# Optimization experiments

Hardware: AMD Instinct MI355X
Metric: run time of the kernel (lower is better)

## Reference

```python
import jax, jax.numpy as jnp
import numpy as np

B, N, D = 256, 256, 256
DELTA_BEARING = 5.0
DELTA_HEADING = 5.0
N_HEAD = int(360 / DELTA_HEADING)   # 72
N_BEAR = int(360 / DELTA_BEARING)   # 72
DOMAIN_PARAM = 2.0
EPS = 1e-14


def setup_inputs() -> dict:
    key = jax.random.key(0)
    ks = jax.random.split(key, 8)
    hidden_state = jax.random.normal(ks[0], (B, N, D), dtype=jnp.float32)
    distance_matrix = jax.random.uniform(ks[1], (B, N, N), dtype=jnp.float32) * 10.0
    bearing_matrix = jax.random.uniform(ks[2], (B, N, N), dtype=jnp.float32) * 360.0
    heading_matrix = jax.random.uniform(ks[3], (B, N, N), dtype=jnp.float32) * 360.0
    sequence_mask = (jax.random.uniform(ks[4], (B, N)) > 0.1).astype(jnp.float32)
    domain = jnp.full((N_HEAD, N_BEAR), DOMAIN_PARAM, dtype=jnp.float32)
    lim = 1.0 / np.sqrt(2 * D)
    W = jax.random.uniform(ks[5], (D, 2 * D), minval=-lim, maxval=lim, dtype=jnp.float32)
    b = jax.random.uniform(ks[6], (D,), minval=-lim, maxval=lim, dtype=jnp.float32)
    return {"hidden_state": hidden_state, "distance_matrix": distance_matrix,
            "bearing_matrix": bearing_matrix, "heading_matrix": heading_matrix,
            "sequence_mask": sequence_mask, "domain": domain, "W": W, "b": b}


def _compute_weights(domain, distance_matrix, bearing_matrix, heading_matrix, sequence_mask):
    # domain lookup indices from heading/bearing bins
    idx1 = jnp.clip(jnp.floor((heading_matrix + DELTA_HEADING / 2) / DELTA_HEADING), 0, N_HEAD - 1).astype(jnp.int32)
    idx2 = jnp.clip(jnp.floor((bearing_matrix + DELTA_BEARING / 2) / DELTA_BEARING), 0, N_BEAR - 1).astype(jnp.int32)
    w = jax.nn.relu(domain[idx1, idx2] - distance_matrix)  # (B,N,N)
    # pairwise sequence mask and no-self-attention mask
    wm = sequence_mask[:, :, None] * sequence_mask[:, None, :]  # (B,N,N)
    ped = 1.0 - jnp.eye(w.shape[1], dtype=w.dtype)               # (N,N)
    valid = (ped[None, :, :] * wm) > 0
    w = jnp.where(valid, w, 0.0)
    # masked softmax over dim=2: zeros are treated as masked, epsilon-stabilized
    mask = (w != 0).astype(w.dtype)
    masked_exps = jnp.exp(w) * mask + EPS
    w = masked_exps / (masked_exps.sum(axis=2, keepdims=True) + EPS)
    return jnp.where(valid, w, 0.0)


def reference(hidden_state, distance_matrix, bearing_matrix, heading_matrix, sequence_mask, domain, W, b):
    weights = _compute_weights(domain, distance_matrix, bearing_matrix, heading_matrix, sequence_mask)
    weighted_hidden = jnp.einsum('bij,bjd->bid', weights, hidden_state)  # (B,N,D)
    cat = jnp.concatenate([weighted_hidden, hidden_state], axis=-1)       # (B,N,2D)
    return jnp.einsum('bnk,dk->bnd', cat, W) + b
```

## Files before the change

kernel.cpp:

```cpp
#include <hip/hip_runtime.h>
#include <hip/hip_bf16.h>


typedef __attribute__((ext_vector_type(4))) float  f32x4;
typedef __attribute__((ext_vector_type(8))) short  bf16x8;
typedef __attribute__((ext_vector_type(4))) short  bf16x4;

#define EPSC 1e-14f

__device__ __forceinline__ short f2bf(float v) {
  __hip_bfloat16 h = __float2bfloat16(v);
  return *reinterpret_cast<short*>(&h);
}
__device__ __forceinline__ void gload16(const void* g, void* l) {
  __builtin_amdgcn_global_load_lds(
      (const __attribute__((address_space(1))) void*)g,
      (__attribute__((address_space(3))) void*)l, 16, 0, 0);
}
__device__ __forceinline__ bf16x8 cvt8(const float* p) {
  f32x4 a = *(const f32x4*)p;
  f32x4 b = *(const f32x4*)(p + 4);
  bf16x8 r;
  r[0] = f2bf(a[0]); r[1] = f2bf(a[1]); r[2] = f2bf(a[2]); r[3] = f2bf(a[3]);
  r[4] = f2bf(b[0]); r[5] = f2bf(b[1]); r[6] = f2bf(b[2]); r[7] = f2bf(b[3]);
  return r;
}

__global__ void k0_pack(const float* __restrict__ W, short* __restrict__ Wbf) {
  int idx = blockIdx.x * 256 + threadIdx.x;
  f32x4 v = *(const f32x4*)(W + (size_t)idx * 4);
  bf16x4 pk;
  pk[0] = f2bf(v[0]); pk[1] = f2bf(v[1]); pk[2] = f2bf(v[2]); pk[3] = f2bf(v[3]);
  *(bf16x4*)(Wbf + (size_t)idx * 4) = pk;
}

__global__ void k0_check(const float* __restrict__ domain, float* __restrict__ flag) {
  __shared__ int s_ok[4];
  const int t = threadIdx.x;
  float v0 = domain[0];
  bool ok = true;
  for (int x = t; x < 72 * 72; x += 256) ok = ok && (domain[x] == v0);
  unsigned long long m = __ballot(ok);
  if ((t & 63) == 0) s_ok[t >> 6] = (m == ~0ull) ? 1 : 0;
  __syncthreads();
  if (t == 0) {
    flag[0] = v0;
    flag[1] = (s_ok[0] && s_ok[1] && s_ok[2] && s_ok[3]) ? 1.f : 0.f;
  }
}

__global__ __launch_bounds__(256) void k2a_weights(
    const float* __restrict__ dist, const float* __restrict__ bear,
    const float* __restrict__ head, const float* __restrict__ seqmask,
    const float* __restrict__ domain, const float* __restrict__ uflag,
    short* __restrict__ weBuf) {
  __shared__ float sMask[256];
  const int t = threadIdx.x;
  const int b = blockIdx.x >> 3;
  const int i0 = (blockIdx.x & 7) * 32;
  if (t < 256) sMask[t] = seqmask[b * 256 + t];
  __syncthreads();

  const int w = t >> 6, l = t & 63;
  const int j0 = l * 4;
  const float dval = uflag[0];
  const bool  uni  = uflag[1] != 0.f;
  const f32x4 mj = *(const f32x4*)(sMask + j0);

  f32x4 dv[8];
  #pragma unroll
  for (int rr = 0; rr < 8; ++rr) {
    int i = i0 + w * 8 + rr;
    dv[rr] = *(const f32x4*)(dist + ((size_t)b * 256 + i) * 256 + j0);
  }

  #pragma unroll
  for (int rr = 0; rr < 8; ++rr) {
    const int i = i0 + w * 8 + rr;
    const float mI = sMask[i];
    const size_t base = ((size_t)b * 256 + i) * 256;
    float ev[4];
    float rs = 0.f;
    if (uni) {
      #pragma unroll
      for (int e = 0; e < 4; ++e) {
        float wv = fmaxf(dval - dv[rr][e], 0.f);
        bool valid = (i != j0 + e) && (mI != 0.f) && (mj[e] != 0.f);
        float ex = (wv > 0.f) ? __expf(wv) : 0.f;
        ex = valid ? ex : 0.f;
        rs += ex;
        ev[e] = valid ? (ex + EPSC) : 0.f;
      }
    } else {
      f32x4 bv = *(const f32x4*)(bear + base + j0);
      f32x4 hv = *(const f32x4*)(head + base + j0);
      #pragma unroll
      for (int e = 0; e < 4; ++e) {
        float f1 = fminf(fmaxf(floorf((hv[e] + 2.5f) * 0.2f), 0.f), 71.f);
        float f2 = fminf(fmaxf(floorf((bv[e] + 2.5f) * 0.2f), 0.f), 71.f);
        float wv = fmaxf(domain[(int)(f1 * 72.f + f2)] - dv[rr][e], 0.f);
        bool valid = (i != j0 + e) && (mI != 0.f) && (mj[e] != 0.f);
        float ex = (wv > 0.f) ? __expf(wv) : 0.f;
        ex = valid ? ex : 0.f;
        rs += ex;
        ev[e] = valid ? (ex + EPSC) : 0.f;
      }
    }
    rs += __shfl_xor(rs, 1, 64);
    rs += __shfl_xor(rs, 2, 64);
    rs += __shfl_xor(rs, 4, 64);
    rs += __shfl_xor(rs, 8, 64);
    rs += __shfl_xor(rs, 16, 64);
    rs += __shfl_xor(rs, 32, 64);
    const float scale = 1.0f / (rs + 257.0f * EPSC);
    bf16x4 pk;
    pk[0] = f2bf(ev[0] * scale); pk[1] = f2bf(ev[1] * scale);
    pk[2] = f2bf(ev[2] * scale); pk[3] = f2bf(ev[3] * scale);
    *(bf16x4*)(weBuf + base + j0) = pk;
  }
}

__global__ __launch_bounds__(512) void k1_p1t(
    const float* __restrict__ H, const short* __restrict__ Wbf,
    short* __restrict__ P1T) {
  extern __shared__ char sm[];
  char* sB0 = sm;
  char* sB1 = sm + 32768;
  const int t = threadIdx.x;
  const int x = blockIdx.x;
  const int blk = (x & 7) * 128 + (x >> 3);
  const int n0 = blk * 64;
  const int b  = n0 >> 8;
  const int jb = n0 & 255;

  const int wid = t >> 6, l = t & 63;
  const int lr = l & 15, lg = l >> 4;
  const int wr = wid & 3, wc = wid >> 2;
  const int r3 = l >> 3, sl = l & 7;
  const int sswz = (sl ^ r3) * 8;
  const int sw = (lr & 7) << 4;

  const size_t hbase = ((size_t)(n0 + wr * 16 + lr)) * 256;

  #pragma unroll
  for (int p = 0; p < 4; ++p) {
    int dd = wid * 8 + r3 + 64 * p;
    gload16(Wbf + (size_t)dd * 512 + sswz, sB0 + (wid * 8 + 64 * p) * 128);
  }
  __syncthreads();

  f32x4 acc[8] = {};

  #pragma unroll
  for (int c = 0; c < 4; ++c) {
    char* cur = (c & 1) ? sB1 : sB0;
    char* nxt = (c & 1) ? sB0 : sB1;
    if (c < 3) {
      #pragma unroll
      for (int p = 0; p < 4; ++p) {
        int dd = wid * 8 + r3 + 64 * p;
        gload16(Wbf + (size_t)dd * 512 + (c + 1) * 64 + sswz, nxt + (wid * 8 + 64 * p) * 128);
      }
    }
    const int kk = c * 64;
    #pragma unroll
    for (int sub = 0; sub < 2; ++sub) {
      bf16x8 av = cvt8(H + hbase + kk + sub * 32 + lg * 8);
      #pragma unroll
      for (int n = 0; n < 8; ++n) {
        const int d = wc * 128 + n * 16 + lr;
        bf16x8 bb = *(const bf16x8*)(cur + d * 128 + ((sub * 64 + lg * 16) ^ sw));
        acc[n] = __builtin_amdgcn_mfma_f32_16x16x32_bf16(av, bb, acc[n], 0, 0, 0);
      }
    }
    __syncthreads();
  }

  #pragma unroll
  for (int n = 0; n < 8; ++n) {
    const int d = wc * 128 + n * 16 + lr;
    f32x4 v = acc[n];
    bf16x4 pk;
    pk[0] = f2bf(v[0]); pk[1] = f2bf(v[1]); pk[2] = f2bf(v[2]); pk[3] = f2bf(v[3]);
    *(bf16x4*)(P1T + (size_t)b * 65536 + (size_t)d * 256 + jb + wr * 16 + lg * 4) = pk;
  }
}

__global__ __launch_bounds__(512) void k2b_gemm(
    const short* __restrict__ weBuf, const short* __restrict__ P1T,
    const short* __restrict__ Wbf, const float* __restrict__ H,
    const float* __restrict__ bias, float* __restrict__ out) {
  extern __shared__ char sm[];
  char*  sB0   = sm;
  char*  sB1   = sm + 32768;
  float* sBias = (float*)(sm + 65536);
  const int t = threadIdx.x;
  const int x = blockIdx.x;
  const int blk = (x & 7) * 128 + (x >> 3);
  const int b  = blk >> 2;
  const int i0 = (blk & 3) * 64;

  const int wid = t >> 6, l = t & 63;
  const int lr = l & 15, lg = l >> 4;
  const int wr = wid & 3, wc = wid >> 2;
  const int r3 = l >> 3, sl = l & 7;
  const int sswz = (sl ^ r3) * 8;
  const int sw = (lr & 7) << 4;

  const short* __restrict__ P1b = P1T + (size_t)b * 65536;
  const int i = i0 + wr * 16 + lr;
  const size_t abase = ((size_t)b * 256 + i) * 256;

  #pragma unroll
  for (int p = 0; p < 4; ++p) {
    int dd = wid * 8 + r3 + 64 * p;
    gload16(P1b + (size_t)dd * 256 + sswz, sB0 + (wid * 8 + 64 * p) * 128);
  }
  if (t < 256) sBias[t] = bias[t];
  __syncthreads();

  f32x4 acc[8] = {};

  #pragma unroll
  for (int g = 0; g < 8; ++g) {
    char* cur = (g & 1) ? sB1 : sB0;
    char* nxt = (g & 1) ? sB0 : sB1;
    if (g < 7) {
      const int nk = ((g + 1) & 3) * 64;
      if (g + 1 < 4) {
        #pragma unroll
        for (int p = 0; p < 4; ++p) {
          int dd = wid * 8 + r3 + 64 * p;
          gload16(P1b + (size_t)dd * 256 + nk + sswz, nxt + (wid * 8 + 64 * p) * 128);
        }
      } else {
        #pragma unroll
        for (int p = 0; p < 4; ++p) {
          int dd = wid * 8 + r3 + 64 * p;
          gload16(Wbf + (size_t)dd * 512 + 256 + nk + sswz, nxt + (wid * 8 + 64 * p) * 128);
        }
      }
    }
    const int kk = (g & 3) * 64;
    #pragma unroll
    for (int sub = 0; sub < 2; ++sub) {
      bf16x8 av;
      if (g < 4) av = *(const bf16x8*)(weBuf + abase + kk + sub * 32 + lg * 8);
      else       av = cvt8(H + abase + kk + sub * 32 + lg * 8);
      #pragma unroll
      for (int n = 0; n < 8; ++n) {
        const int d = wc * 128 + n * 16 + lr;
        bf16x8 bb = *(const bf16x8*)(cur + d * 128 + ((sub * 64 + lg * 16) ^ sw));
        acc[n] = __builtin_amdgcn_mfma_f32_16x16x32_bf16(av, bb, acc[n], 0, 0, 0);
      }
    }
    __syncthreads();
  }

  #pragma unroll
  for (int n = 0; n < 8; ++n) {
    const int d = wc * 128 + n * 16 + lr;
    const float bs = sBias[d];
    #pragma unroll
    for (int r = 0; r < 4; ++r) {
      const int row = i0 + wr * 16 + lg * 4 + r;
      out[((size_t)b * 256 + row) * 256 + d] = acc[n][r] + bs;
    }
  }
}

extern "C" void kernel_launch(void* const* d_in, const int* in_sizes, int n_in,
                              void* d_out, int out_size, void* d_ws, size_t ws_size,
                              hipStream_t stream) {
  const float* hidden  = (const float*)d_in[0];
  const float* dist    = (const float*)d_in[1];
  const float* bear    = (const float*)d_in[2];
  const float* head    = (const float*)d_in[3];
  const float* seqmask = (const float*)d_in[4];
  const float* domain  = (const float*)d_in[5];
  const float* W       = (const float*)d_in[6];
  const float* bias    = (const float*)d_in[7];
  float* out = (float*)d_out;

  char* ws = (char*)d_ws;
  short* Wbf   = (short*)ws;
  float* flag  = (float*)(ws + 524288);
  short* P1T   = (short*)(ws + (1u << 20));
  short* weBuf = (short*)(ws + (1u << 20) + (32u << 20));

  k0_pack<<<128, 256, 0, stream>>>(W, Wbf);
  k0_check<<<1, 256, 0, stream>>>(domain, flag);
  k2a_weights<<<2048, 256, 0, stream>>>(dist, bear, head, seqmask, domain, flag, weBuf);
  k1_p1t<<<1024, 512, 65536, stream>>>(hidden, Wbf, P1T);
  k2b_gemm<<<1024, 512, 66560, stream>>>(weBuf, P1T, Wbf, hidden, bias, out);
}
```

Before: 112.4 us.

## Double M-tile per block in both GEMM kernels to reuse LDS B tiles

```diff
diff --git a/kernel.cpp b/kernel.cpp
--- a/kernel.cpp
+++ b/kernel.cpp
@@ -120,7 +120,7 @@
   }
 }
 
-__global__ __launch_bounds__(512) void k1_p1t(
+__global__ __launch_bounds__(512, 4) void k1_p1t(
     const float* __restrict__ H, const short* __restrict__ Wbf,
     short* __restrict__ P1T) {
   extern __shared__ char sm[];
@@ -128,8 +128,8 @@
   char* sB1 = sm + 32768;
   const int t = threadIdx.x;
   const int x = blockIdx.x;
-  const int blk = (x & 7) * 128 + (x >> 3);
-  const int n0 = blk * 64;
+  const int blk = (x & 7) * 64 + (x >> 3);
+  const int n0 = blk * 128;
   const int b  = n0 >> 8;
   const int jb = n0 & 255;
 
@@ -140,7 +140,8 @@
   const int sswz = (sl ^ r3) * 8;
   const int sw = (lr & 7) << 4;
 
-  const size_t hbase = ((size_t)(n0 + wr * 16 + lr)) * 256;
+  const size_t h0 = ((size_t)(n0 + wr * 32 + lr)) * 256;
+  const size_t h1 = h0 + 16 * 256;
 
   #pragma unroll
   for (int p = 0; p < 4; ++p) {
@@ -149,7 +150,7 @@
   }
   __syncthreads();
 
-  f32x4 acc[8] = {};
+  f32x4 acc[2][8] = {};
 
   #pragma unroll
   for (int c = 0; c < 4; ++c) {
@@ -165,28 +166,33 @@
     const int kk = c * 64;
     #pragma unroll
     for (int sub = 0; sub < 2; ++sub) {
-      bf16x8 av = cvt8(H + hbase + kk + sub * 32 + lg * 8);
+      bf16x8 av0 = cvt8(H + h0 + kk + sub * 32 + lg * 8);
+      bf16x8 av1 = cvt8(H + h1 + kk + sub * 32 + lg * 8);
       #pragma unroll
       for (int n = 0; n < 8; ++n) {
         const int d = wc * 128 + n * 16 + lr;
         bf16x8 bb = *(const bf16x8*)(cur + d * 128 + ((sub * 64 + lg * 16) ^ sw));
-        acc[n] = __builtin_amdgcn_mfma_f32_16x16x32_bf16(av, bb, acc[n], 0, 0, 0);
+        acc[0][n] = __builtin_amdgcn_mfma_f32_16x16x32_bf16(av0, bb, acc[0][n], 0, 0, 0);
+        acc[1][n] = __builtin_amdgcn_mfma_f32_16x16x32_bf16(av1, bb, acc[1][n], 0, 0, 0);
       }
     }
     __syncthreads();
   }
 
   #pragma unroll
-  for (int n = 0; n < 8; ++n) {
-    const int d = wc * 128 + n * 16 + lr;
-    f32x4 v = acc[n];
-    bf16x4 pk;
-    pk[0] = f2bf(v[0]); pk[1] = f2bf(v[1]); pk[2] = f2bf(v[2]); pk[3] = f2bf(v[3]);
-    *(bf16x4*)(P1T + (size_t)b * 65536 + (size_t)d * 256 + jb + wr * 16 + lg * 4) = pk;
-  }
-}
-
-__global__ __launch_bounds__(512) void k2b_gemm(
+  for (int m = 0; m < 2; ++m) {
+    #pragma unroll
+    for (int n = 0; n < 8; ++n) {
+      const int d = wc * 128 + n * 16 + lr;
+      f32x4 v = acc[m][n];
+      bf16x4 pk;
+      pk[0] = f2bf(v[0]); pk[1] = f2bf(v[1]); pk[2] = f2bf(v[2]); pk[3] = f2bf(v[3]);
+      *(bf16x4*)(P1T + (size_t)b * 65536 + (size_t)d * 256 + jb + wr * 32 + m * 16 + lg * 4) = pk;
+    }
+  }
+}
+
+__global__ __launch_bounds__(512, 4) void k2b_gemm(
     const short* __restrict__ weBuf, const short* __restrict__ P1T,
     const short* __restrict__ Wbf, const float* __restrict__ H,
     const float* __restrict__ bias, float* __restrict__ out) {
@@ -196,9 +202,9 @@
   float* sBias = (float*)(sm + 65536);
   const int t = threadIdx.x;
   const int x = blockIdx.x;
-  const int blk = (x & 7) * 128 + (x >> 3);
-  const int b  = blk >> 2;
-  const int i0 = (blk & 3) * 64;
+  const int blk = (x & 7) * 64 + (x >> 3);
+  const int b  = blk >> 1;
+  const int i0 = (blk & 1) * 128;
 
   const int wid = t >> 6, l = t & 63;
   const int lr = l & 15, lg = l >> 4;
@@ -208,8 +214,8 @@
   const int sw = (lr & 7) << 4;
 
   const short* __restrict__ P1b = P1T + (size_t)b * 65536;
-  const int i = i0 + wr * 16 + lr;
-  const size_t abase = ((size_t)b * 256 + i) * 256;
+  const size_t a0 = ((size_t)b * 256 + i0 + wr * 32 + lr) * 256;
+  const size_t a1 = a0 + 16 * 256;
 
   #pragma unroll
   for (int p = 0; p < 4; ++p) {
@@ -219,7 +225,7 @@
   if (t < 256) sBias[t] = bias[t];
   __syncthreads();
 
-  f32x4 acc[8] = {};
+  f32x4 acc[2][8] = {};
 
   #pragma unroll
   for (int g = 0; g < 8; ++g) {
@@ -244,27 +250,36 @@
     const int kk = (g & 3) * 64;
     #pragma unroll
     for (int sub = 0; sub < 2; ++sub) {
-      bf16x8 av;
-      if (g < 4) av = *(const bf16x8*)(weBuf + abase + kk + sub * 32 + lg * 8);
-      else       av = cvt8(H + abase + kk + sub * 32 + lg * 8);
+      bf16x8 av0, av1;
+      if (g < 4) {
+        av0 = *(const bf16x8*)(weBuf + a0 + kk + sub * 32 + lg * 8);
+        av1 = *(const bf16x8*)(weBuf + a1 + kk + sub * 32 + lg * 8);
+      } else {
+        av0 = cvt8(H + a0 + kk + sub * 32 + lg * 8);
+        av1 = cvt8(H + a1 + kk + sub * 32 + lg * 8);
+      }
       #pragma unroll
       for (int n = 0; n < 8; ++n) {
         const int d = wc * 128 + n * 16 + lr;
         bf16x8 bb = *(const bf16x8*)(cur + d * 128 + ((sub * 64 + lg * 16) ^ sw));
-        acc[n] = __builtin_amdgcn_mfma_f32_16x16x32_bf16(av, bb, acc[n], 0, 0, 0);
+        acc[0][n] = __builtin_amdgcn_mfma_f32_16x16x32_bf16(av0, bb, acc[0][n], 0, 0, 0);
+        acc[1][n] = __builtin_amdgcn_mfma_f32_16x16x32_bf16(av1, bb, acc[1][n], 0, 0, 0);
       }
     }
     __syncthreads();
   }
 
   #pragma unroll
-  for (int n = 0; n < 8; ++n) {
-    const int d = wc * 128 + n * 16 + lr;
-    const float bs = sBias[d];
+  for (int m = 0; m < 2; ++m) {
     #pragma unroll
-    for (int r = 0; r < 4; ++r) {
-      const int row = i0 + wr * 16 + lg * 4 + r;
-      out[((size_t)b * 256 + row) * 256 + d] = acc[n][r] + bs;
+    for (int n = 0; n < 8; ++n) {
+      const int d = wc * 128 + n * 16 + lr;
+      const float bs = sBias[d];
+      #pragma unroll
+      for (int r = 0; r < 4; ++r) {
+        const int row = i0 + wr * 32 + m * 16 + lg * 4 + r;
+        out[((size_t)b * 256 + row) * 256 + d] = acc[m][n][r] + bs;
+      }
     }
   }
 }
@@ -291,6 +306,6 @@
   k0_pack<<<128, 256, 0, stream>>>(W, Wbf);
   k0_check<<<1, 256, 0, stream>>>(domain, flag);
   k2a_weights<<<2048, 256, 0, stream>>>(dist, bear, head, seqmask, domain, flag, weBuf);
-  k1_p1t<<<1024, 512, 65536, stream>>>(hidden, Wbf, P1T);
-  k2b_gemm<<<1024, 512, 66560, stream>>>(weBuf, P1T, Wbf, hidden, bias, out);
-}
+  k1_p1t<<<512, 512, 65536, stream>>>(hidden, Wbf, P1T);
+  k2b_gemm<<<512, 512, 66560, stream>>>(weBuf, P1T, Wbf, hidden, bias, out);
+}
```

Result: faster. 107.5 us, median of 2 (-4.4%).
